# Performance work log

Measured on AMD Instinct MI355X. Metric: run time of the kernel, lower is better.

## Reference

```python
import jax, jax.numpy as jnp
import numpy as np

B = 4096
NQ = 4  # qubits -> 16-dim state vector


def _make_ops(seed, n_ops):
    # Deterministic stand-in for tq.RandomLayer: random RX/RY/RZ/CRX gates.
    rng = np.random.default_rng(seed)
    ops = []
    for _ in range(n_ops):
        kind = int(rng.integers(0, 4))
        if kind == 3:  # CRX on two distinct wires
            w = rng.choice(NQ, size=2, replace=False)
            ops.append((3, int(w[0]), int(w[1])))
        else:
            ops.append((kind, int(rng.integers(0, NQ)), 0))
    return ops

ENC_OPS = _make_ops(1, 8)    # QuantumPatchEncoder.random_layer (n_ops=8)
QFC_OPS = _make_ops(2, 50)   # QuantumFullyConnectedLayer.random_layer (n_ops=50)

_H = np.array([[1, 1], [1, -1]], np.complex64) * np.complex64(1.0 / np.sqrt(2.0))
_SX = np.array([[1 + 1j, 1 - 1j], [1 - 1j, 1 + 1j]], np.complex64) * np.complex64(0.5)
_CNOT = np.array([[1, 0, 0, 0], [0, 1, 0, 0], [0, 0, 0, 1], [0, 0, 1, 0]], np.complex64)


def _rx(t):
    c = jnp.cos(t / 2) + 0j
    s = -1j * jnp.sin(t / 2)
    return jnp.stack([jnp.stack([c, s], -1), jnp.stack([s, c], -1)], -2)


def _ry(t):
    c = jnp.cos(t / 2) + 0j
    s = jnp.sin(t / 2) + 0j
    return jnp.stack([jnp.stack([c, -s], -1), jnp.stack([s, c], -1)], -2)


def _rz(t):
    e0 = jnp.exp(-1j * t / 2)
    e1 = jnp.exp(1j * t / 2)
    z = jnp.zeros_like(e0)
    return jnp.stack([jnp.stack([e0, z], -1), jnp.stack([z, e1], -1)], -2)


def _crx(t):
    return jnp.eye(4, dtype=jnp.complex64).at[2:, 2:].set(_rx(t))


def _apply1(state, U, w):
    # state: (B, 2,2,2,2); U: (2,2) or per-sample (B,2,2)
    state = jnp.moveaxis(state, w + 1, -1)
    if U.ndim == 3:
        state = jnp.einsum('b...i,bji->b...j', state, U)
    else:
        state = jnp.einsum('...i,ji->...j', state, U)
    return jnp.moveaxis(state, -1, w + 1)


def _apply2(state, U, w0, w1):
    state = jnp.moveaxis(state, (w0 + 1, w1 + 1), (-2, -1))
    shp = state.shape
    state = state.reshape(shp[:-2] + (4,)) @ U.T
    return jnp.moveaxis(state.reshape(shp), (-2, -1), (w0 + 1, w1 + 1))


def _random_layer(state, ops, params):
    for i, (kind, w0, w1) in enumerate(ops):
        t = params[i]
        if kind == 0:
            state = _apply1(state, _rx(t), w0)
        elif kind == 1:
            state = _apply1(state, _ry(t), w0)
        elif kind == 2:
            state = _apply1(state, _rz(t), w0)
        else:
            state = _apply2(state, _crx(t), w0, w1)
    return state


def _measure_z(state):
    # <Z> on each wire from |amp|^2 marginals
    probs = state.real ** 2 + state.imag ** 2
    exps = []
    for w in range(NQ):
        axes = tuple(a for a in range(1, NQ + 1) if a != w + 1)
        m = probs.sum(axes)  # (B, 2)
        exps.append(m[:, 0] - m[:, 1])
    return jnp.stack(exps, 1)


def _conv(x, W, b):
    y = jax.lax.conv_general_dilated(x, W, (1, 1), 'SAME',
                                     dimension_numbers=('NCHW', 'OIHW', 'NCHW'))
    return y + b[None, :, None, None]


def _pool(x):
    return jax.lax.reduce_window(x, -jnp.inf, jax.lax.max,
                                 (1, 1, 2, 2), (1, 1, 2, 2), 'VALID')


def setup_inputs() -> dict:
    key = jax.random.key(0)
    ks = jax.random.split(key, 8)
    f = lambda k, shp, fan: jax.random.normal(k, shp, jnp.float32) / np.float32(np.sqrt(fan))
    two_pi = float(2 * np.pi)
    return {
        'x': jax.random.uniform(ks[0], (B, 1, 32, 32), jnp.float32),
        'conv1_w': f(ks[1], (8, 1, 3, 3), 9),
        'conv1_b': jnp.zeros((8,), jnp.float32),
        'conv2_w': f(ks[2], (16, 8, 3, 3), 72),
        'conv2_b': jnp.zeros((16,), jnp.float32),
        'enc_params': jax.random.uniform(ks[3], (8,), jnp.float32, 0.0, two_pi),
        'qfc_rand_params': jax.random.uniform(ks[4], (50,), jnp.float32, 0.0, two_pi),
        'qfc_params': jax.random.uniform(ks[5], (4,), jnp.float32, 0.0, two_pi),
        'bn_gamma': jnp.ones((4,), jnp.float32),
        'bn_beta': jnp.zeros((4,), jnp.float32),
        'fc_w': f(ks[6], (10, 68), 68),
        'fc_b': jnp.zeros((10,), jnp.float32),
    }


def reference(x, conv1_w, conv1_b, conv2_w, conv2_b, enc_params, qfc_rand_params,
              qfc_params, bn_gamma, bn_beta, fc_w, fc_b):
    # CNN feature extractor
    h = _pool(jax.nn.relu(_conv(x, conv1_w, conv1_b)))
    h = _pool(jax.nn.relu(_conv(h, conv2_w, conv2_b)))  # (B, 16, 8, 8)
    b = h.shape[0]
    pm = h.mean(1)  # channel-mean, (B, 8, 8)
    # 2x2 patches, row-major within patch, scanning r then c -> (B, 16, 4)
    patches = pm.reshape(b, 4, 2, 4, 2).transpose(0, 1, 3, 2, 4).reshape(b, 16, 4)

    # Encoder: fresh |0000> per patch (GeneralEncoder resets state); batch all
    # B*16 patch circuits together instead of looping.
    data = patches.reshape(b * 16, 4)
    state = jnp.zeros((b * 16, 16), jnp.complex64).at[:, 0].set(1.0)
    state = state.reshape(b * 16, 2, 2, 2, 2)
    for w in range(NQ):
        state = _apply1(state, _ry(data[:, w]), w)
    state = _random_layer(state, ENC_OPS, enc_params)
    qfeat = _measure_z(state).reshape(b, 64)  # (B, 16*4)

    # QFC operates on the state left by the LAST patch (as in the original)
    s = state.reshape(b, 16, 2, 2, 2, 2)[:, 15]
    s = _random_layer(s, QFC_OPS, qfc_rand_params)
    s = _apply1(s, _rx(qfc_params[0]), 0)
    s = _apply1(s, _ry(qfc_params[1]), 1)
    s = _apply1(s, _rz(qfc_params[2]), 3)
    s = _apply2(s, _crx(qfc_params[3]), 0, 2)
    s = _apply1(s, jnp.asarray(_H), 3)
    s = _apply1(s, jnp.asarray(_SX), 2)
    s = _apply2(s, jnp.asarray(_CNOT), 3, 0)
    q = _measure_z(s)  # (B, 4)

    # BatchNorm1d(4), training-mode (batch stats, biased var)
    mu = q.mean(0)
    var = q.var(0)
    q = (q - mu) / jnp.sqrt(var + 1e-5) * bn_gamma + bn_beta

    feats = jnp.concatenate([qfeat, q], 1)  # (B, 68)
    logits = feats @ fc_w.T + fc_b
    return jax.nn.log_softmax(logits, -1)
```

## Files before the change

### kernel.cpp

```cpp
#include <hip/hip_runtime.h>
#include <cstdint>

namespace crng {

typedef unsigned __int128 u128;

struct PCG {
    u128 state, inc;
    bool has32;
    uint32_t buf32;
};

constexpr u128 PCG_MULT = (((u128)2549297995355413924ULL) << 64) | (u128)4865540595714422341ULL;

constexpr uint64_t pcg_next64(PCG& g) {
    g.state = g.state * PCG_MULT + g.inc;
    uint64_t hi = (uint64_t)(g.state >> 64), lo = (uint64_t)g.state;
    unsigned rot = (unsigned)(g.state >> 122) & 63u;
    uint64_t v = hi ^ lo;
    return (v >> rot) | (v << ((64u - rot) & 63u));
}

constexpr uint32_t pcg_next32(PCG& g) {
    if (g.has32) { g.has32 = false; return g.buf32; }
    uint64_t n = pcg_next64(g);
    g.has32 = true;
    g.buf32 = (uint32_t)(n >> 32);
    return (uint32_t)n;
}

constexpr uint32_t hashmix(uint32_t& hc, uint32_t v) {
    v ^= hc; hc *= 0x931e8875u; v *= hc; v ^= v >> 16; return v;
}
constexpr uint32_t mixf(uint32_t x, uint32_t y) {
    uint32_t r = 0xca01f9ddu * x - 0x4973f715u * y;
    r ^= r >> 16;
    return r;
}

constexpr PCG seed_pcg(uint32_t entropy) {
    uint32_t pool[4] = {0, 0, 0, 0};
    uint32_t hc = 0x43b0d7e5u;
    pool[0] = hashmix(hc, entropy);
    for (int i = 1; i < 4; ++i) pool[i] = hashmix(hc, 0u);
    for (int s = 0; s < 4; ++s)
        for (int d = 0; d < 4; ++d)
            if (s != d) pool[d] = mixf(pool[d], hashmix(hc, pool[s]));

    uint32_t hb = 0x8b51f9ddu;
    uint32_t w[8] = {0, 0, 0, 0, 0, 0, 0, 0};
    for (int i = 0; i < 8; ++i) {
        uint32_t dv = pool[i & 3];
        dv ^= hb; hb *= 0x58f38dedu; dv *= hb; dv ^= dv >> 16;
        w[i] = dv;
    }
    uint64_t w64[4] = {0, 0, 0, 0};
    for (int i = 0; i < 4; ++i)
        w64[i] = (uint64_t)w[2 * i] | ((uint64_t)w[2 * i + 1] << 32);

    u128 initstate = (((u128)w64[0]) << 64) | (u128)w64[1];
    u128 initseq   = (((u128)w64[2]) << 64) | (u128)w64[3];
    PCG g = {};
    g.state = 0;
    g.inc = (initseq << 1) | (u128)1;
    g.state = g.state * PCG_MULT + g.inc;
    g.state += initstate;
    g.state = g.state * PCG_MULT + g.inc;
    g.has32 = false;
    g.buf32 = 0;
    return g;
}

constexpr uint32_t lemire32(PCG& g, uint32_t rng) {
    uint64_t rng_excl = (uint64_t)rng + 1;
    uint64_t m = (uint64_t)pcg_next32(g) * rng_excl;
    uint32_t leftover = (uint32_t)m;
    if (leftover < (uint32_t)rng_excl) {
        uint32_t threshold = (uint32_t)((uint64_t)(0xFFFFFFFFu - rng) % rng_excl);
        while (leftover < threshold) {
            m = (uint64_t)pcg_next32(g) * rng_excl;
            leftover = (uint32_t)m;
        }
    }
    return (uint32_t)(m >> 32);
}

struct Ops {
    int enc[8];
    int qfc[50];
};

constexpr void fill_ops(PCG& g, int n, int* out) {
    for (int i = 0; i < n; ++i) {
        uint32_t kind = lemire32(g, 3);
        uint32_t w0 = 0, w1 = 0;
        if (kind == 3) {
            uint32_t v2 = lemire32(g, 2);
            uint32_t v3 = lemire32(g, 3);
            uint32_t a0 = v2;
            uint32_t a1 = (v3 == v2) ? 3u : v3;
            uint32_t j = lemire32(g, 1);
            if (j == 0) { uint32_t t = a0; a0 = a1; a1 = t; }
            w0 = a0; w1 = a1;
        } else {
            w0 = lemire32(g, 3);
        }
        out[i] = (int)((kind << 4) | (w0 << 2) | w1);
    }
}

constexpr Ops make_ops_ct() {
    Ops o = {};
    PCG g1 = seed_pcg(1u);
    fill_ops(g1, 8, o.enc);
    PCG g2 = seed_pcg(2u);
    fill_ops(g2, 50, o.qfc);
    return o;
}

}

constexpr crng::Ops kOps = crng::make_ops_ct();

#define XS_STRIDE 24
#define XS_PLANE  (34 * XS_STRIDE)
#define XS_TOT    (2 * XS_PLANE)
#define H1_STRIDE 10
#define H1_PLANE  (18 * H1_STRIDE)
#define H1_TOT    (16 * H1_PLANE)

__global__ __launch_bounds__(256, 4) void cnn_kernel(
    const float* __restrict__ x, const float* __restrict__ w1,
    const float* __restrict__ b1, const float* __restrict__ w2,
    const float* __restrict__ b2, float* __restrict__ pm,
    float* __restrict__ stats)
{
    __shared__ float xs[XS_TOT];
    __shared__ float h1s[H1_TOT];
    __shared__ float w1s[72], b1s[8], w2s[1152], b2s[16];
    __shared__ float part[256];

    const int tid = threadIdx.x;
    const int b = blockIdx.x;
    const float* xb = x + (size_t)b * 1024;

    for (int k = tid; k < XS_TOT; k += 256) xs[k] = 0.f;
    for (int k = tid; k < H1_TOT; k += 256) h1s[k] = 0.f;
    for (int k = tid; k < 1152; k += 256) w2s[k] = w2[k];
    if (tid < 72) w1s[tid] = w1[tid];
    if (tid < 8) b1s[tid] = b1[tid];
    if (tid < 16) b2s[tid] = b2[tid];
    if (b == 0 && tid < 8) stats[tid] = 0.f;
    __syncthreads();

    for (int k = tid; k < 1024; k += 256) {
        int r = k >> 5, c = k & 31;
        int p = c & 1;
        int q = p ? ((c + 1) >> 1) : (c >> 1);
        xs[p * XS_PLANE + (r + 1) * XS_STRIDE + q] = xb[k];
    }
    __syncthreads();

    {
        const int i = tid >> 4, j = tid & 15;
        float patch[4][4];
#pragma unroll
        for (int u = 0; u < 4; ++u) {
            int r = 2 * i + u;
            const float* ev = &xs[r * XS_STRIDE + j];
            const float* od = &xs[XS_PLANE + r * XS_STRIDE + j];
            patch[u][0] = od[0];
            patch[u][1] = ev[0];
            patch[u][2] = od[1];
            patch[u][3] = ev[1];
        }
        const int p = j & 1;
        const int q = p ? ((j + 1) >> 1) : (j >> 1);
#pragma unroll
        for (int c = 0; c < 8; ++c) {
            float m = -3.4e38f;
#pragma unroll
            for (int di = 0; di < 2; ++di)
#pragma unroll
                for (int dj = 0; dj < 2; ++dj) {
                    float acc = b1s[c];
#pragma unroll
                    for (int u = 0; u < 3; ++u)
#pragma unroll
                        for (int v = 0; v < 3; ++v)
                            acc += w1s[c * 9 + u * 3 + v] * patch[di + u][dj + v];
                    m = fmaxf(m, acc);
                }
            h1s[(c * 2 + p) * H1_PLANE + (i + 1) * H1_STRIDE + q] = fmaxf(m, 0.f);
        }
    }
    __syncthreads();

    {
        const int pos = tid & 63, cb = tid >> 6;
        const int i2 = pos >> 3, j2 = pos & 7;
        float acc[4][2][2];
#pragma unroll
        for (int k = 0; k < 4; ++k) {
            float bb = b2s[cb * 4 + k];
            acc[k][0][0] = bb; acc[k][0][1] = bb; acc[k][1][0] = bb; acc[k][1][1] = bb;
        }
#pragma unroll
        for (int ci = 0; ci < 8; ++ci) {
            float patch[4][4];
#pragma unroll
            for (int u = 0; u < 4; ++u) {
                int r = 2 * i2 + u;
                const float* ev = &h1s[(ci * 2 + 0) * H1_PLANE + r * H1_STRIDE + j2];
                const float* od = &h1s[(ci * 2 + 1) * H1_PLANE + r * H1_STRIDE + j2];
                patch[u][0] = od[0];
                patch[u][1] = ev[0];
                patch[u][2] = od[1];
                patch[u][3] = ev[1];
            }
#pragma unroll
            for (int k = 0; k < 4; ++k) {
                const float* wp = &w2s[((cb * 4 + k) * 8 + ci) * 9];
#pragma unroll
                for (int di = 0; di < 2; ++di)
#pragma unroll
                    for (int dj = 0; dj < 2; ++dj)
#pragma unroll
                        for (int u = 0; u < 3; ++u)
#pragma unroll
                            for (int v = 0; v < 3; ++v)
                                acc[k][di][dj] += wp[u * 3 + v] * patch[di + u][dj + v];
            }
        }
        float sum = 0.f;
#pragma unroll
        for (int k = 0; k < 4; ++k) {
            float m = fmaxf(fmaxf(acc[k][0][0], acc[k][0][1]),
                            fmaxf(acc[k][1][0], acc[k][1][1]));
            sum += fmaxf(m, 0.f);
        }
        part[cb * 64 + pos] = sum;
    }
    __syncthreads();
    if (tid < 64) {
        float s = part[tid] + part[64 + tid] + part[128 + tid] + part[192 + tid];
        pm[(size_t)b * 64 + tid] = s * (1.f / 16.f);
    }
}

template<int KIND, int W0, int W1>
__device__ __forceinline__ void gate_ct(float (&ur)[16], float (&ui)[16],
                                        float ch, float sh)
{
    constexpr bool CTRL = (KIND == 3 || KIND == 6);
    constexpr int STT = CTRL ? (8 >> W1) : (8 >> W0);
    constexpr int STC = CTRL ? (8 >> W0) : 0;
#pragma unroll
    for (int k0 = 0; k0 < 16; ++k0) {
        if (k0 & STT) continue;
        if (STC != 0 && !(k0 & STC)) continue;
        const int k1 = k0 | STT;
        float x0r = ur[k0], x0i = ui[k0], x1r = ur[k1], x1i = ui[k1];
        if constexpr (KIND == 0 || KIND == 3) {
            ur[k0] = ch * x0r + sh * x1i;  ui[k0] = ch * x0i - sh * x1r;
            ur[k1] = sh * x0i + ch * x1r;  ui[k1] = -sh * x0r + ch * x1i;
        } else if constexpr (KIND == 1) {
            ur[k0] = ch * x0r - sh * x1r;  ui[k0] = ch * x0i - sh * x1i;
            ur[k1] = sh * x0r + ch * x1r;  ui[k1] = sh * x0i + ch * x1i;
        } else if constexpr (KIND == 2) {
            ur[k0] = ch * x0r + sh * x0i;  ui[k0] = ch * x0i - sh * x0r;
            ur[k1] = ch * x1r - sh * x1i;  ui[k1] = ch * x1i + sh * x1r;
        } else if constexpr (KIND == 4) {
            constexpr float RH = 0.70710678118654752f;
            ur[k0] = RH * (x0r + x1r);  ui[k0] = RH * (x0i + x1i);
            ur[k1] = RH * (x0r - x1r);  ui[k1] = RH * (x0i - x1i);
        } else if constexpr (KIND == 5) {
            ur[k0] = 0.5f * (x0r + x1r) - 0.5f * x0i + 0.5f * x1i;
            ui[k0] = 0.5f * (x0i + x1i) + 0.5f * x0r - 0.5f * x1r;
            ur[k1] = 0.5f * (x0r + x1r) + 0.5f * x0i - 0.5f * x1i;
            ui[k1] = 0.5f * (x0i + x1i) - 0.5f * x0r + 0.5f * x1r;
        } else {
            ur[k0] = x1r; ui[k0] = x1i;
            ur[k1] = x0r; ui[k1] = x0i;
        }
    }
}

template<int I>
__device__ __forceinline__ void run_enc(float (&ur)[16], float (&ui)[16],
                                        const float* ch, const float* sh)
{
    if constexpr (I < 8) {
        constexpr int op = kOps.enc[I];
        gate_ct<(op >> 4) & 7, (op >> 2) & 3, op & 3>(ur, ui, ch[I], sh[I]);
        run_enc<I + 1>(ur, ui, ch, sh);
    }
}

template<int I>
__device__ __forceinline__ void run_qfc(float (&ur)[16], float (&ui)[16],
                                        const float* ch, const float* sh)
{
    if constexpr (I < 50) {
        constexpr int op = kOps.qfc[I];
        gate_ct<(op >> 4) & 7, (op >> 2) & 3, op & 3>(ur, ui, ch[I], sh[I]);
        run_qfc<I + 1>(ur, ui, ch, sh);
    }
}

__global__ __launch_bounds__(256) void quantum_kernel(
    const float* __restrict__ pm, const float* __restrict__ encp,
    const float* __restrict__ qfcr, const float* __restrict__ qfcp,
    float* __restrict__ qfeat, float* __restrict__ qraw,
    float* __restrict__ stats, int Bv)
{
    __shared__ float chs[62], shs[62];
    __shared__ float rstat[128];

    const int tid = threadIdx.x;
    if (tid < 62) {
        float t = (tid < 8) ? encp[tid] : (tid < 58) ? qfcr[tid - 8] : qfcp[tid - 58];
        chs[tid] = cosf(0.5f * t);
        shs[tid] = sinf(0.5f * t);
    }
    __syncthreads();

    const int gid = blockIdx.x * 256 + tid;
    const int b = gid >> 4, p = gid & 15;
    float qq[4] = {0.f, 0.f, 0.f, 0.f};
    bool last = false;

    if (b < Bv) {
        const int pr = p >> 2, pc = p & 3;
        const float* pmb = pm + (size_t)b * 64;
        float d0 = pmb[(2 * pr) * 8 + 2 * pc];
        float d1 = pmb[(2 * pr) * 8 + 2 * pc + 1];
        float d2 = pmb[(2 * pr + 1) * 8 + 2 * pc];
        float d3 = pmb[(2 * pr + 1) * 8 + 2 * pc + 1];
        float f0c = cosf(0.5f * d0), f0s = sinf(0.5f * d0);
        float f1c = cosf(0.5f * d1), f1s = sinf(0.5f * d1);
        float f2c = cosf(0.5f * d2), f2s = sinf(0.5f * d2);
        float f3c = cosf(0.5f * d3), f3s = sinf(0.5f * d3);

        float ur[16], ui[16];
#pragma unroll
        for (int k = 0; k < 16; ++k) {
            float v = ((k & 8) ? f0s : f0c);
            v *= ((k & 4) ? f1s : f1c);
            v *= ((k & 2) ? f2s : f2c);
            v *= ((k & 1) ? f3s : f3c);
            ur[k] = v;
            ui[k] = 0.f;
        }
        run_enc<0>(ur, ui, chs, shs);

        float qv[4] = {0.f, 0.f, 0.f, 0.f};
#pragma unroll
        for (int k = 0; k < 16; ++k) {
            float pk = ur[k] * ur[k] + ui[k] * ui[k];
            qv[0] += (k & 8) ? -pk : pk;
            qv[1] += (k & 4) ? -pk : pk;
            qv[2] += (k & 2) ? -pk : pk;
            qv[3] += (k & 1) ? -pk : pk;
        }
        *(float4*)(qfeat + (size_t)b * 64 + p * 4) = make_float4(qv[0], qv[1], qv[2], qv[3]);

        if (p == 15) {
            last = true;
            run_qfc<0>(ur, ui, chs + 8, shs + 8);
            gate_ct<0, 0, 0>(ur, ui, chs[58], shs[58]);
            gate_ct<1, 1, 0>(ur, ui, chs[59], shs[59]);
            gate_ct<2, 3, 0>(ur, ui, chs[60], shs[60]);
            gate_ct<3, 0, 2>(ur, ui, chs[61], shs[61]);
            gate_ct<4, 3, 0>(ur, ui, 0.f, 0.f);
            gate_ct<5, 2, 0>(ur, ui, 0.f, 0.f);
            gate_ct<6, 3, 0>(ur, ui, 0.f, 0.f);
#pragma unroll
            for (int k = 0; k < 16; ++k) {
                float pk = ur[k] * ur[k] + ui[k] * ui[k];
                qq[0] += (k & 8) ? -pk : pk;
                qq[1] += (k & 4) ? -pk : pk;
                qq[2] += (k & 2) ? -pk : pk;
                qq[3] += (k & 1) ? -pk : pk;
            }
            *(float4*)(qraw + (size_t)b * 4) = make_float4(qq[0], qq[1], qq[2], qq[3]);
        }
    }

    for (int k = tid; k < 128; k += 256) rstat[k] = 0.f;
    __syncthreads();
    const int m = tid >> 4;
    if (last) {
#pragma unroll
        for (int w = 0; w < 4; ++w) {
            rstat[w * 16 + m] = qq[w];
            rstat[64 + w * 16 + m] = qq[w] * qq[w];
        }
    }
    __syncthreads();
    if (tid < 8) {
        float s = 0.f;
#pragma unroll
        for (int k = 0; k < 16; ++k) s += rstat[tid * 16 + k];
        atomicAdd(&stats[tid], s);
    }
}

__global__ __launch_bounds__(256) void head_kernel(
    const float* __restrict__ qfeat, const float* __restrict__ qraw,
    const float* __restrict__ stats, const float* __restrict__ gam,
    const float* __restrict__ bet, const float* __restrict__ fcw,
    const float* __restrict__ fcb, float* __restrict__ out, int Bv)
{
    __shared__ float Wf[680];
    __shared__ float bf[10], st[8], ga[4], be[4];
    const int tid = threadIdx.x;
    for (int k = tid; k < 680; k += 256) Wf[k] = fcw[k];
    if (tid < 10) bf[tid] = fcb[tid];
    if (tid < 8) st[tid] = stats[tid];
    if (tid < 4) { ga[tid] = gam[tid]; be[tid] = bet[tid]; }
    __syncthreads();

    const int b = blockIdx.x * 256 + tid;
    if (b >= Bv) return;

    const float invB = 1.f / (float)Bv;

    float logit[10];
#pragma unroll
    for (int k = 0; k < 10; ++k) logit[k] = bf[k];

    const float* qf = qfeat + (size_t)b * 64;
    for (int j = 0; j < 64; ++j) {
        float v = qf[j];
#pragma unroll
        for (int k = 0; k < 10; ++k) logit[k] += v * Wf[k * 68 + j];
    }
    float4 qr = *(const float4*)(qraw + (size_t)b * 4);
    float qn[4] = {qr.x, qr.y, qr.z, qr.w};
#pragma unroll
    for (int w = 0; w < 4; ++w) {
        float mu = st[w] * invB;
        float var = st[4 + w] * invB - mu * mu;
        float v = (qn[w] - mu) / sqrtf(var + 1e-5f) * ga[w] + be[w];
#pragma unroll
        for (int k = 0; k < 10; ++k) logit[k] += v * Wf[k * 68 + 64 + w];
    }

    float m = logit[0];
#pragma unroll
    for (int k = 1; k < 10; ++k) m = fmaxf(m, logit[k]);
    float sum = 0.f;
#pragma unroll
    for (int k = 0; k < 10; ++k) sum += expf(logit[k] - m);
    float lse = logf(sum);
#pragma unroll
    for (int k = 0; k < 10; ++k) out[(size_t)b * 10 + k] = logit[k] - m - lse;
}

extern "C" void kernel_launch(void* const* d_in, const int* in_sizes, int n_in,
                              void* d_out, int out_size, void* d_ws, size_t ws_size,
                              hipStream_t stream)
{
    const float* x    = (const float*)d_in[0];
    const float* w1   = (const float*)d_in[1];
    const float* b1   = (const float*)d_in[2];
    const float* w2   = (const float*)d_in[3];
    const float* b2   = (const float*)d_in[4];
    const float* encp = (const float*)d_in[5];
    const float* qfcr = (const float*)d_in[6];
    const float* qfcp = (const float*)d_in[7];
    const float* gam  = (const float*)d_in[8];
    const float* bet  = (const float*)d_in[9];
    const float* fcw  = (const float*)d_in[10];
    const float* fcb  = (const float*)d_in[11];
    float* out = (float*)d_out;

    const int Bv = in_sizes[0] / 1024;

    float* pm    = (float*)d_ws;
    float* qfeat = pm + (size_t)Bv * 64;
    float* qraw  = qfeat + (size_t)Bv * 64;
    float* stats = qraw + (size_t)Bv * 4;

    cnn_kernel<<<Bv, 256, 0, stream>>>(x, w1, b1, w2, b2, pm, stats);
    quantum_kernel<<<(Bv * 16 + 255) / 256, 256, 0, stream>>>(
        pm, encp, qfcr, qfcp, qfeat, qraw, stats, Bv);
    head_kernel<<<(Bv + 255) / 256, 256, 0, stream>>>(qfeat, qraw, stats, gam, bet,
                                                      fcw, fcb, out, Bv);
}
```

Measured before the change: 157.5 us.

## Run second convolution on MFMA f16 matrix cores with channel-interleaved layout

Replaces the scalar FP32 second conv layer with MFMA 16x16x32 f16 instructions. The first conv output is stored in LDS as fp16 with channels packed contiguously per pixel, and weights are repacked to fp16 A fragments. Pooling and the channel sum are done with cross-lane shuffles instead of a shared partial buffer and an extra barrier. This trades FP32 accuracy for fp16 inputs and wastes part of the K dimension, since only one quad carries nonzero A data.

```diff
diff --git a/kernel.cpp b/kernel.cpp
--- a/kernel.cpp
+++ b/kernel.cpp
@@ -122,12 +122,13 @@
 
 constexpr crng::Ops kOps = crng::make_ops_ct();
 
+typedef _Float16 half8 __attribute__((ext_vector_type(8)));
+typedef float float4v __attribute__((ext_vector_type(4)));
+
 #define XS_STRIDE 24
 #define XS_PLANE  (34 * XS_STRIDE)
 #define XS_TOT    (2 * XS_PLANE)
-#define H1_STRIDE 10
-#define H1_PLANE  (18 * H1_STRIDE)
-#define H1_TOT    (16 * H1_PLANE)
+#define H1F_ROW   (18 * 8)
 
 __global__ __launch_bounds__(256, 4) void cnn_kernel(
     const float* __restrict__ x, const float* __restrict__ w1,
@@ -136,17 +137,20 @@
     float* __restrict__ stats)
 {
     __shared__ float xs[XS_TOT];
-    __shared__ float h1s[H1_TOT];
-    __shared__ float w1s[72], b1s[8], w2s[1152], b2s[16];
-    __shared__ float part[256];
+    __shared__ __align__(16) _Float16 h1f[18 * H1F_ROW];
+    __shared__ __align__(16) _Float16 Ahalf[9 * 16 * 8];
+    __shared__ float w1s[72], b1s[8], b2s[16];
 
     const int tid = threadIdx.x;
     const int b = blockIdx.x;
     const float* xb = x + (size_t)b * 1024;
 
     for (int k = tid; k < XS_TOT; k += 256) xs[k] = 0.f;
-    for (int k = tid; k < H1_TOT; k += 256) h1s[k] = 0.f;
-    for (int k = tid; k < 1152; k += 256) w2s[k] = w2[k];
+    for (int k = tid; k < 18 * H1F_ROW; k += 256) h1f[k] = (_Float16)0.f;
+    for (int e = tid; e < 1152; e += 256) {
+        int uv = e >> 7, m = (e >> 3) & 15, ci = e & 7;
+        Ahalf[e] = (_Float16)w2[m * 72 + ci * 9 + uv];
+    }
     if (tid < 72) w1s[tid] = w1[tid];
     if (tid < 8) b1s[tid] = b1[tid];
     if (tid < 16) b2s[tid] = b2[tid];
@@ -174,8 +178,7 @@
             patch[u][2] = od[1];
             patch[u][3] = ev[1];
         }
-        const int p = j & 1;
-        const int q = p ? ((j + 1) >> 1) : (j >> 1);
+        half8 hv;
 #pragma unroll
         for (int c = 0; c < 8; ++c) {
             float m = -3.4e38f;
@@ -191,60 +194,69 @@
                             acc += w1s[c * 9 + u * 3 + v] * patch[di + u][dj + v];
                     m = fmaxf(m, acc);
                 }
-            h1s[(c * 2 + p) * H1_PLANE + (i + 1) * H1_STRIDE + q] = fmaxf(m, 0.f);
-        }
+            hv[c] = (_Float16)fmaxf(m, 0.f);
+        }
+        *(half8*)&h1f[(i + 1) * H1F_ROW + (j + 1) * 8] = hv;
     }
     __syncthreads();
 
     {
-        const int pos = tid & 63, cb = tid >> 6;
-        const int i2 = pos >> 3, j2 = pos & 7;
-        float acc[4][2][2];
-#pragma unroll
-        for (int k = 0; k < 4; ++k) {
-            float bb = b2s[cb * 4 + k];
-            acc[k][0][0] = bb; acc[k][0][1] = bb; acc[k][1][0] = bb; acc[k][1][1] = bb;
-        }
-#pragma unroll
-        for (int ci = 0; ci < 8; ++ci) {
-            float patch[4][4];
-#pragma unroll
-            for (int u = 0; u < 4; ++u) {
-                int r = 2 * i2 + u;
-                const float* ev = &h1s[(ci * 2 + 0) * H1_PLANE + r * H1_STRIDE + j2];
-                const float* od = &h1s[(ci * 2 + 1) * H1_PLANE + r * H1_STRIDE + j2];
-                patch[u][0] = od[0];
-                patch[u][1] = ev[0];
-                patch[u][2] = od[1];
-                patch[u][3] = ev[1];
+        const int w = tid >> 6;
+        const int lane = tid & 63;
+        const int pj = lane & 15;
+        const int quad = lane >> 4;
+
+        half8 afrag[9];
+#pragma unroll
+        for (int uv = 0; uv < 9; ++uv) {
+            half8 a = {};
+            if (quad == 0) a = *(const half8*)&Ahalf[(uv * 16 + pj) * 8];
+            afrag[uv] = a;
+        }
+
+        float4v acc[4];
+#pragma unroll
+        for (int tl = 0; tl < 4; ++tl) {
+            float4v c;
+#pragma unroll
+            for (int r = 0; r < 4; ++r) c[r] = b2s[4 * quad + r];
+            acc[tl] = c;
+        }
+
+#pragma unroll
+        for (int tl = 0; tl < 4; ++tl) {
+            const int t = 4 * w + tl;
+#pragma unroll
+            for (int u = 0; u < 3; ++u) {
+#pragma unroll
+                for (int v = 0; v < 3; ++v) {
+                    half8 bf = *(const half8*)&h1f[(t + u) * H1F_ROW + (pj + v) * 8];
+                    acc[tl] = __builtin_amdgcn_mfma_f32_16x16x32_f16(
+                        afrag[u * 3 + v], bf, acc[tl], 0, 0, 0);
+                }
             }
-#pragma unroll
-            for (int k = 0; k < 4; ++k) {
-                const float* wp = &w2s[((cb * 4 + k) * 8 + ci) * 9];
-#pragma unroll
-                for (int di = 0; di < 2; ++di)
-#pragma unroll
-                    for (int dj = 0; dj < 2; ++dj)
-#pragma unroll
-                        for (int u = 0; u < 3; ++u)
-#pragma unroll
-                            for (int v = 0; v < 3; ++v)
-                                acc[k][di][dj] += wp[u * 3 + v] * patch[di + u][dj + v];
+        }
+
+#pragma unroll
+        for (int p = 0; p < 2; ++p) {
+            float4v m1;
+#pragma unroll
+            for (int r = 0; r < 4; ++r)
+                m1[r] = fmaxf(acc[2 * p][r], acc[2 * p + 1][r]);
+            float s = 0.f;
+#pragma unroll
+            for (int r = 0; r < 4; ++r) {
+                float o = __shfl_xor((float)m1[r], 1, 64);
+                float mv = fmaxf(fmaxf(m1[r], o), 0.f);
+                s += mv;
             }
-        }
-        float sum = 0.f;
-#pragma unroll
-        for (int k = 0; k < 4; ++k) {
-            float m = fmaxf(fmaxf(acc[k][0][0], acc[k][0][1]),
-                            fmaxf(acc[k][1][0], acc[k][1][1]));
-            sum += fmaxf(m, 0.f);
-        }
-        part[cb * 64 + pos] = sum;
-    }
-    __syncthreads();
-    if (tid < 64) {
-        float s = part[tid] + part[64 + tid] + part[128 + tid] + part[192 + tid];
-        pm[(size_t)b * 64 + tid] = s * (1.f / 16.f);
+            s += __shfl_xor(s, 16, 64);
+            s += __shfl_xor(s, 32, 64);
+            if (quad == 0 && !(pj & 1)) {
+                const int i2 = 2 * w + p, j2 = pj >> 1;
+                pm[(size_t)b * 64 + i2 * 8 + j2] = s * (1.f / 16.f);
+            }
+        }
     }
 }
 
```

New measurement: 139.3 us, median of 2. 11.6% less time.
